# Kernel optimization log

Hardware: AMD Instinct MI355X
Metric: run time of the kernel (lower is better)

Reference implementation:

```python
import jax, jax.numpy as jnp
import numpy as np

IN_F = 4096
OUT_F = 4096
BW = 8
RNG_LEN = 2 ** BW  # 256


def _sobol_1d(bw):
    # 1-D Sobol sequence == van der Corput (bit-reversed) integers in [0, 2^bw),
    # matching UnarySim's RNG(bitwidth, 1, 'Sobol') table.
    n = 2 ** bw
    idx = np.arange(n, dtype=np.int64)
    rev = np.zeros(n, dtype=np.int64)
    for b in range(bw):
        rev |= ((idx >> b) & 1) << (bw - 1 - b)
    return rev.astype(np.float32)


def setup_inputs() -> dict:
    key = jax.random.key(0)
    k1, k2, k3, k4, k5, k6 = jax.random.split(key, 6)
    # unary (bit-serial) input bits for one clock cycle, batch=1
    x = jax.random.randint(k1, (1, IN_F), 0, 2).astype(jnp.float32)
    # SourceGen output: integer comparison thresholds in [0, 2^bw), stored as float
    buf_wght = jax.random.randint(k2, (OUT_F, IN_F), 0, RNG_LEN).astype(jnp.float32)
    buf_bias = jax.random.randint(k3, (OUT_F,), 0, RNG_LEN).astype(jnp.float32)
    rng = jnp.asarray(_sobol_1d(BW))  # [256] Sobol table
    # persistent BSGen index state (mid-stream snapshot, values in [0, 256))
    rng_wght_idx = jax.random.randint(k4, (OUT_F, IN_F), 0, RNG_LEN).astype(jnp.int64)
    rng_bias_idx = jax.random.randint(k5, (OUT_F,), 0, RNG_LEN).astype(jnp.int64)
    rng_wght_idx_inv = jax.random.randint(k6, (OUT_F, IN_F), 0, RNG_LEN).astype(jnp.int64)
    # persistent output accumulator (broadcast to [1, out] after first call)
    acc = jnp.zeros((1, OUT_F), dtype=jnp.float32)
    acc_bound = jnp.full((1,), float(IN_F + 1), dtype=jnp.float32)  # in_features + 1 (bias)
    return {"x": x, "buf_wght": buf_wght, "buf_bias": buf_bias, "rng": rng,
            "acc": acc, "acc_bound": acc_bound,
            "rng_wght_idx": rng_wght_idx, "rng_bias_idx": rng_bias_idx,
            "rng_wght_idx_inv": rng_wght_idx_inv}


def reference(x, buf_wght, buf_bias, rng, acc, acc_bound,
              rng_wght_idx, rng_bias_idx, rng_wght_idx_inv):
    L = rng.shape[0]
    # BSGen: regenerate binarized weight/bias bits via indexed gather + compare
    w_bit = (buf_wght >= rng[rng_wght_idx % L]).astype(jnp.float32)      # [out, in]
    b_bit = (buf_bias >= rng[rng_bias_idx % L]).astype(jnp.float32)      # [out]
    kernel_out = x @ w_bit.T + b_bit                                     # [1, out]
    # bipolar inverse path: inverted bits applied to inverted input
    w_bit_inv = 1.0 - (buf_wght >= rng[rng_wght_idx_inv % L]).astype(jnp.float32)
    kernel_out_inv = (1.0 - x) @ w_bit_inv.T                             # [1, out]
    # scaled accumulate-and-threshold
    acc_new = acc + kernel_out + kernel_out_inv
    out = (acc_new >= acc_bound).astype(jnp.float32)                     # [1, out]
    return out
```

## Files before the change

kernel.cpp:

```cpp
#include <hip/hip_runtime.h>
#include <stdint.h>


constexpr int IN_F  = 4096;
constexpr int OUT_F = 4096;

__device__ __forceinline__ float contrib(float w, int ii, int vi, float xf) {
    const float r  = (float)(__brev((unsigned)ii) >> 24);
    const float ri = (float)(__brev((unsigned)vi) >> 24);
    return (xf != 0.0f) ? ((w >= r) ? 1.0f : 0.0f)
                        : ((w >= ri) ? 0.0f : 1.0f);
}

#define GLOAD_LDS16(gp, lp)                                                  \
    __builtin_amdgcn_global_load_lds(                                        \
        (const __attribute__((address_space(1))) void*)(gp),                 \
        (__attribute__((address_space(3))) void*)(lp), 16, 0, 0)

__global__ __launch_bounds__(256) void unary_linear_kernel(
    const float* __restrict__ x,
    const float* __restrict__ buf_wght,
    const float* __restrict__ buf_bias,
    const float* __restrict__ acc,
    const float* __restrict__ acc_bound,
    const int*   __restrict__ rng_wght_idx,
    const int*   __restrict__ rng_bias_idx,
    const int*   __restrict__ rng_wght_idx_inv,
    float*       __restrict__ out)
{
    const int row  = blockIdx.x;
    const int tid  = threadIdx.x;
    const int wave = tid >> 6;
    const int lane = tid & 63;

    __shared__ float lds_w[IN_F];
    __shared__ int   lds_i[IN_F];
    __shared__ int   lds_v[IN_F];
    __shared__ float wsum[4];

    const char* wrow = (const char*)(buf_wght         + (size_t)row * IN_F);
    const char* irow = (const char*)(rng_wght_idx     + (size_t)row * IN_F);
    const char* vrow = (const char*)(rng_wght_idx_inv + (size_t)row * IN_F);

    #pragma unroll
    for (int c = 0; c < 4; ++c) {
        const int ch   = wave * 4 + c;
        const int goff = ch * 1024 + lane * 16;
        const int loff = ch * 1024;
        GLOAD_LDS16(wrow + goff, (char*)lds_w + loff);
        GLOAD_LDS16(irow + goff, (char*)lds_i + loff);
        GLOAD_LDS16(vrow + goff, (char*)lds_v + loff);
    }

    __syncthreads();

    float sum = 0.0f;
    #pragma unroll
    for (int c = 0; c < 16; ++c) {
        const int e = c * 256 + tid;
        sum += contrib(lds_w[e], lds_i[e], lds_v[e], x[e]);
    }

    #pragma unroll
    for (int off = 32; off > 0; off >>= 1)
        sum += __shfl_down(sum, off);

    if (lane == 0) wsum[wave] = sum;
    __syncthreads();

    if (tid == 0) {
        const float rb = (float)(__brev((unsigned)rng_bias_idx[row]) >> 24);
        const float b_bit = (buf_bias[row] >= rb) ? 1.0f : 0.0f;
        const float total = acc[row] + wsum[0] + wsum[1] + wsum[2] + wsum[3] + b_bit;
        out[row] = (total >= acc_bound[0]) ? 1.0f : 0.0f;
    }
}

extern "C" void kernel_launch(void* const* d_in, const int* in_sizes, int n_in,
                              void* d_out, int out_size, void* d_ws, size_t ws_size,
                              hipStream_t stream)
{
    const float* x         = (const float*)d_in[0];
    const float* buf_wght  = (const float*)d_in[1];
    const float* buf_bias  = (const float*)d_in[2];
    const float* acc       = (const float*)d_in[4];
    const float* acc_bound = (const float*)d_in[5];
    const int*   rwi       = (const int*)d_in[6];
    const int*   rbi       = (const int*)d_in[7];
    const int*   rwii      = (const int*)d_in[8];
    float* out = (float*)d_out;

    dim3 grid(OUT_F);
    dim3 block(256);
    hipLaunchKernelGGL(unary_linear_kernel, grid, block, 0, stream,
                       x, buf_wght, buf_bias, acc, acc_bound,
                       rwi, rbi, rwii, out);
}
```

Before: 230.2 us.

## Stream rows via nontemporal vector loads, two rows per block with XCD-aware mapping

Drops the LDS staging of weight and index rows. Each thread now issues 16-byte nontemporal vector loads straight into registers, and x is held in registers across rows. Each block handles two rows, with row assignment swizzled so that each XCD works on a contiguous range of rows, and the grid is halved. The goal is to remove LDS round-trips and barriers on a purely bandwidth-bound stream, at the cost of less latency hiding per block, since there is no async prefetch and two serial rows each take their own barriers.

```diff
diff --git a/kernel.cpp b/kernel.cpp
--- a/kernel.cpp
+++ b/kernel.cpp
@@ -4,6 +4,10 @@
 
 constexpr int IN_F  = 4096;
 constexpr int OUT_F = 4096;
+constexpr int NXCD  = 8;
+
+typedef float v4f __attribute__((ext_vector_type(4)));
+typedef int   v4i __attribute__((ext_vector_type(4)));
 
 __device__ __forceinline__ float contrib(float w, int ii, int vi, float xf) {
     const float r  = (float)(__brev((unsigned)ii) >> 24);
@@ -12,12 +16,7 @@
                         : ((w >= ri) ? 0.0f : 1.0f);
 }
 
-#define GLOAD_LDS16(gp, lp)                                                  \
-    __builtin_amdgcn_global_load_lds(                                        \
-        (const __attribute__((address_space(1))) void*)(gp),                 \
-        (__attribute__((address_space(3))) void*)(lp), 16, 0, 0)
-
-__global__ __launch_bounds__(256) void unary_linear_kernel(
+__global__ __launch_bounds__(256, 4) void unary_linear_kernel(
     const float* __restrict__ x,
     const float* __restrict__ buf_wght,
     const float* __restrict__ buf_bias,
@@ -28,51 +27,57 @@
     const int*   __restrict__ rng_wght_idx_inv,
     float*       __restrict__ out)
 {
-    const int row  = blockIdx.x;
     const int tid  = threadIdx.x;
     const int wave = tid >> 6;
     const int lane = tid & 63;
 
-    __shared__ float lds_w[IN_F];
-    __shared__ int   lds_i[IN_F];
-    __shared__ int   lds_v[IN_F];
+    const int xcd  = blockIdx.x & (NXCD - 1);
+    const int slot = blockIdx.x >> 3;
+    const int row0 = xcd * (OUT_F / NXCD) + slot * 2;
+
     __shared__ float wsum[4];
 
-    const char* wrow = (const char*)(buf_wght         + (size_t)row * IN_F);
-    const char* irow = (const char*)(rng_wght_idx     + (size_t)row * IN_F);
-    const char* vrow = (const char*)(rng_wght_idx_inv + (size_t)row * IN_F);
+    v4f xv[4];
+    #pragma unroll
+    for (int i = 0; i < 4; ++i)
+        xv[i] = *reinterpret_cast<const v4f*>(x + (i * 256 + tid) * 4);
 
     #pragma unroll
-    for (int c = 0; c < 4; ++c) {
-        const int ch   = wave * 4 + c;
-        const int goff = ch * 1024 + lane * 16;
-        const int loff = ch * 1024;
-        GLOAD_LDS16(wrow + goff, (char*)lds_w + loff);
-        GLOAD_LDS16(irow + goff, (char*)lds_i + loff);
-        GLOAD_LDS16(vrow + goff, (char*)lds_v + loff);
-    }
+    for (int rr = 0; rr < 2; ++rr) {
+        const int row = row0 + rr;
+        const float* __restrict__ wrow = buf_wght         + (size_t)row * IN_F;
+        const int*   __restrict__ irow = rng_wght_idx     + (size_t)row * IN_F;
+        const int*   __restrict__ vrow = rng_wght_idx_inv + (size_t)row * IN_F;
 
-    __syncthreads();
+        float sum = 0.0f;
+        #pragma unroll
+        for (int i = 0; i < 4; ++i) {
+            const int base = (i * 256 + tid) * 4;
+            const v4f w  = __builtin_nontemporal_load(
+                               reinterpret_cast<const v4f*>(wrow + base));
+            const v4i ii = __builtin_nontemporal_load(
+                               reinterpret_cast<const v4i*>(irow + base));
+            const v4i vi = __builtin_nontemporal_load(
+                               reinterpret_cast<const v4i*>(vrow + base));
+            sum += contrib(w.x, ii.x, vi.x, xv[i].x)
+                 + contrib(w.y, ii.y, vi.y, xv[i].y)
+                 + contrib(w.z, ii.z, vi.z, xv[i].z)
+                 + contrib(w.w, ii.w, vi.w, xv[i].w);
+        }
 
-    float sum = 0.0f;
-    #pragma unroll
-    for (int c = 0; c < 16; ++c) {
-        const int e = c * 256 + tid;
-        sum += contrib(lds_w[e], lds_i[e], lds_v[e], x[e]);
-    }
+        #pragma unroll
+        for (int off = 32; off > 0; off >>= 1)
+            sum += __shfl_down(sum, off);
 
-    #pragma unroll
-    for (int off = 32; off > 0; off >>= 1)
-        sum += __shfl_down(sum, off);
-
-    if (lane == 0) wsum[wave] = sum;
-    __syncthreads();
-
-    if (tid == 0) {
-        const float rb = (float)(__brev((unsigned)rng_bias_idx[row]) >> 24);
-        const float b_bit = (buf_bias[row] >= rb) ? 1.0f : 0.0f;
-        const float total = acc[row] + wsum[0] + wsum[1] + wsum[2] + wsum[3] + b_bit;
-        out[row] = (total >= acc_bound[0]) ? 1.0f : 0.0f;
+        if (lane == 0) wsum[wave] = sum;
+        __syncthreads();
+        if (tid == 0) {
+            const float rb = (float)(__brev((unsigned)rng_bias_idx[row]) >> 24);
+            const float b_bit = (buf_bias[row] >= rb) ? 1.0f : 0.0f;
+            const float total = acc[row] + wsum[0] + wsum[1] + wsum[2] + wsum[3] + b_bit;
+            out[row] = (total >= acc_bound[0]) ? 1.0f : 0.0f;
+        }
+        __syncthreads();
     }
 }
 
@@ -90,7 +95,7 @@
     const int*   rwii      = (const int*)d_in[8];
     float* out = (float*)d_out;
 
-    dim3 grid(OUT_F);
+    dim3 grid(2048);
     dim3 block(256);
     hipLaunchKernelGGL(unary_linear_kernel, grid, block, 0, stream,
                        x, buf_wght, buf_bias, acc, acc_bound,
```

Result: faster. 195.8 us (-14.9%).
